# Kernel tuning notes

Hardware: AMD Instinct MI355X
Metric: run time of the kernel (lower is better)

The kernel has to match this reference:

```python
import jax, jax.numpy as jnp
import numpy as np

B, E, H, W = 8, 256, 128, 128
E0 = E1 = E2 = E3 = E // 4  # channel_split=[2,2,2,2] -> equal quarters


def _dwconv(x, w, b, dilation, padding):
    # x: [B,C,H,W], w: [C,1,kh,kw] (OIHW, feature_group_count=C), b: [C]
    C = x.shape[1]
    y = jax.lax.conv_general_dilated(
        x, w,
        window_strides=(1, 1),
        padding=[(padding, padding), (padding, padding)],
        rhs_dilation=(dilation, dilation),
        feature_group_count=C,
        dimension_numbers=("NCHW", "OIHW", "NCHW"))
    return y + b[None, :, None, None]


def setup_inputs() -> dict:
    key = jax.random.key(0)
    ks = jax.random.split(key, 9)
    s = 0.05
    return {
        "x": jax.random.normal(ks[0], (B, E, H, W), dtype=jnp.float32),
        "w0": jax.random.normal(ks[1], (E, 1, 3, 3), dtype=jnp.float32) * s,
        "b0": jax.random.normal(ks[2], (E,), dtype=jnp.float32) * s,
        "w1": jax.random.normal(ks[3], (E1, 1, 3, 3), dtype=jnp.float32) * s,
        "b1": jax.random.normal(ks[4], (E1,), dtype=jnp.float32) * s,
        "w2": jax.random.normal(ks[5], (E2, 1, 5, 5), dtype=jnp.float32) * s,
        "b2": jax.random.normal(ks[6], (E2,), dtype=jnp.float32) * s,
        "w_pw": jax.random.normal(ks[7], (E, E), dtype=jnp.float32) * s,
        "b_pw": jax.random.normal(ks[8], (E,), dtype=jnp.float32) * s,
    }


def reference(x, w0, b0, w1, b1, w2, b2, w_pw, b_pw):
    # Stage 1: full-width 3x3 depthwise, dilation 1, padding 1
    x0 = _dwconv(x, w0, b0, dilation=1, padding=1)
    # Branch convs on channel slices of x0 (note: original code applies
    # DW_conv2 to BOTH the 3rd and 4th slices; DW_conv3 is never used).
    x1 = _dwconv(x0[:, E0:E0 + E1], w1, b1, dilation=3, padding=3)          # 3x3 dil3
    x2 = _dwconv(x0[:, E0 + E1:E0 + E1 + E2], w2, b2, dilation=3, padding=6)  # 5x5 dil3
    x3 = _dwconv(x0[:, E - E3:], w2, b2, dilation=3, padding=6)             # reuses DW_conv2
    xc = jnp.concatenate([x0[:, :E0], x1, x2, x3], axis=1)  # [B,E,H,W]
    # 1x1 pointwise conv as a channel GEMM
    y = jnp.einsum("bchw,oc->bohw", xc, w_pw) + b_pw[None, :, None, None]
    return y
```

## Files before the change

kernel.cpp:

```cpp
#include <hip/hip_runtime.h>

typedef _Float16 f16;
typedef _Float16 f16x8 __attribute__((ext_vector_type(8)));
typedef unsigned short u16x8 __attribute__((ext_vector_type(8)));
typedef float f32x4 __attribute__((ext_vector_type(4)));

#define GLB_AS(p) ((const __attribute__((address_space(1))) unsigned int*)(p))
#define LDS_AS(p) ((__attribute__((address_space(3))) unsigned int*)(p))

__global__ __launch_bounds__(256) void whalf(const float* __restrict__ w,
                                             f16* __restrict__ wh) {
  int i = blockIdx.x * 256 + threadIdx.x;
  wh[i] = (f16)w[i];
}

template <int HT>
__global__ __launch_bounds__(256) void dwfuse(
    const float* __restrict__ x, const float* __restrict__ w0,
    const float* __restrict__ b0, const float* __restrict__ w1,
    const float* __restrict__ b1, const float* __restrict__ w2,
    const float* __restrict__ b2, f16* __restrict__ Xp) {
  constexpr int S2 = 32 + 2 * HT;
  constexpr int S1 = S2 + 2;
  constexpr int PO = (HT == 6) ? 2 : 0;
  constexpr int QW = (S2 + 3) / 4;
  __shared__ float xs[S1 * 48];
  __shared__ float ts[S2 * 48];
  const int tid = threadIdx.x;

  int b, ch;
  if constexpr (HT == 0) { b = blockIdx.z >> 6; ch = (int)(blockIdx.z & 63); }
  else if constexpr (HT == 3) { b = blockIdx.z >> 6; ch = 64 + (int)(blockIdx.z & 63); }
  else { b = blockIdx.z >> 7; ch = 128 + (int)(blockIdx.z & 127); }
  const int plane = b * 256 + ch;
  const int R0 = (int)blockIdx.y * 32, C0 = (int)blockIdx.x * 32;
  const float* xp = x + (size_t)plane * 16384;

  float W0[9];
#pragma unroll
  for (int k = 0; k < 9; ++k) W0[k] = w0[ch * 9 + k];
  const float B0 = b0[ch];

  const int br = R0 - HT - 1, bc = C0 - HT - 1;
  for (int i = tid; i < S1 * S1; i += 256) {
    int r = i / S1, c = i - r * S1;
    int gr = br + r, gc = bc + c;
    float v = 0.f;
    if ((unsigned)gr < 128u && (unsigned)gc < 128u) v = xp[gr * 128 + gc];
    xs[r * 48 + c] = v;
  }
  __syncthreads();

  for (int q = tid; q < S2 * QW; q += 256) {
    int r = q / QW, c4 = (q - r * QW) * 4;
    float a0 = 0, a1 = 0, a2 = 0, a3 = 0;
#pragma unroll
    for (int dy = 0; dy < 3; ++dy) {
      const float* row = &xs[(r + dy) * 48 + c4];
      float4 qa = *(const float4*)row;
      float4 qb = *(const float4*)(row + 4);
      float wA = W0[dy * 3 + 0], wB = W0[dy * 3 + 1], wC = W0[dy * 3 + 2];
      a0 += wA * qa.x + wB * qa.y + wC * qa.z;
      a1 += wA * qa.y + wB * qa.z + wC * qa.w;
      a2 += wA * qa.z + wB * qa.w + wC * qb.x;
      a3 += wA * qa.w + wB * qb.x + wC * qb.y;
    }
    int gr = R0 - HT + r;
    int gc = C0 - HT + c4;
    bool rok = (unsigned)gr < 128u;
    float o0 = (rok && (unsigned)(gc + 0) < 128u) ? a0 + B0 : 0.f;
    float o1 = (rok && (unsigned)(gc + 1) < 128u) ? a1 + B0 : 0.f;
    float o2 = (rok && (unsigned)(gc + 2) < 128u) ? a2 + B0 : 0.f;
    float o3 = (rok && (unsigned)(gc + 3) < 128u) ? a3 + B0 : 0.f;
    float* tp = &ts[r * 48 + c4 + PO];
    tp[0] = o0; tp[1] = o1; tp[2] = o2; tp[3] = o3;
  }
  __syncthreads();

  const int orow = tid >> 3;
  const int oc4 = (tid & 7) << 2;
  float o0, o1, o2, o3;
  if constexpr (HT == 0) {
    float4 qa = *(const float4*)&ts[orow * 48 + oc4];
    o0 = qa.x; o1 = qa.y; o2 = qa.z; o3 = qa.w;
  } else if constexpr (HT == 3) {
    const int wi = ch & 63;
    float W1[9];
#pragma unroll
    for (int k = 0; k < 9; ++k) W1[k] = w1[wi * 9 + k];
    o0 = o1 = o2 = o3 = b1[wi];
#pragma unroll
    for (int dy = 0; dy < 3; ++dy) {
      const float* row = &ts[(orow + 3 * dy) * 48 + oc4];
      float4 qa = *(const float4*)row;
      float4 qb = *(const float4*)(row + 4);
      float4 qc = *(const float4*)(row + 8);
      float v[12] = {qa.x, qa.y, qa.z, qa.w, qb.x, qb.y, qb.z, qb.w,
                     qc.x, qc.y, qc.z, qc.w};
#pragma unroll
      for (int dx = 0; dx < 3; ++dx) {
        float w = W1[dy * 3 + dx];
        o0 += w * v[3 * dx + 0];
        o1 += w * v[3 * dx + 1];
        o2 += w * v[3 * dx + 2];
        o3 += w * v[3 * dx + 3];
      }
    }
  } else {
    const int wi = ch & 63;
    float W2[25];
#pragma unroll
    for (int k = 0; k < 25; ++k) W2[k] = w2[wi * 25 + k];
    o0 = o1 = o2 = o3 = b2[wi];
#pragma unroll
    for (int dy = 0; dy < 5; ++dy) {
      const float* row = &ts[(orow + 3 * dy) * 48 + oc4];
      float4 qa = *(const float4*)(row + 0);
      float4 qb = *(const float4*)(row + 4);
      float4 qc = *(const float4*)(row + 8);
      float4 qd = *(const float4*)(row + 12);
      float4 qe = *(const float4*)(row + 16);
      float v[20] = {qa.x, qa.y, qa.z, qa.w, qb.x, qb.y, qb.z, qb.w,
                     qc.x, qc.y, qc.z, qc.w, qd.x, qd.y, qd.z, qd.w,
                     qe.x, qe.y, qe.z, qe.w};
#pragma unroll
      for (int dx = 0; dx < 5; ++dx) {
        float w = W2[dy * 5 + dx];
        o0 += w * v[3 * dx + 2];
        o1 += w * v[3 * dx + 3];
        o2 += w * v[3 * dx + 4];
        o3 += w * v[3 * dx + 5];
      }
    }
  }
  const size_t oidx =
      (size_t)plane * 16384 + (size_t)(R0 + orow) * 128 + (C0 + oc4);
  union { f16 h[4]; uint2 u; } ph;
  ph.h[0] = (f16)o0; ph.h[1] = (f16)o1; ph.h[2] = (f16)o2; ph.h[3] = (f16)o3;
  *(uint2*)&Xp[oidx] = ph.u;
}

__global__ __launch_bounds__(256) void t_xpose(const f16* __restrict__ Xp,
                                               f16* __restrict__ XT) {
  __shared__ unsigned ld[64 * 65];
  const int t = threadIdx.x;
  const int b = (int)blockIdx.z, c0 = (int)blockIdx.y << 6,
            p0 = (int)blockIdx.x << 6;
  {
    const int r = t >> 2, ch = (t & 3) << 4;
    const f16* src = Xp + (((size_t)b * 256 + c0 + r) << 14) + p0 + ch;
    u16x8 v0 = *(const u16x8*)src;
    u16x8 v1 = *(const u16x8*)(src + 8);
#pragma unroll
    for (int i = 0; i < 8; ++i) ld[r * 65 + ch + i] = v0[i];
#pragma unroll
    for (int i = 0; i < 8; ++i) ld[r * 65 + ch + 8 + i] = v1[i];
  }
  __syncthreads();
  {
    const int pr = t >> 2, cc = (t & 3) << 4;
    u16x8 w0, w1;
#pragma unroll
    for (int i = 0; i < 8; ++i) w0[i] = (unsigned short)ld[(cc + i) * 65 + pr];
#pragma unroll
    for (int i = 0; i < 8; ++i)
      w1[i] = (unsigned short)ld[(cc + 8 + i) * 65 + pr];
    f16* dst = XT + (((size_t)b * 16384 + p0 + pr) << 8) + c0 + cc;
    *(u16x8*)dst = w0;
    *(u16x8*)(dst + 8) = w1;
  }
}

__global__ __launch_bounds__(256) void pwgemm(const f16* __restrict__ XT,
                                              const f16* __restrict__ Wh,
                                              const float* __restrict__ bpw,
                                              float* __restrict__ out) {
  __shared__ f16 smem[4096];
  const int tid = threadIdx.x, lane = tid & 63, wid = tid >> 6;
  const int bx = (int)blockIdx.x;
  const int nblk = bx >> 1;
  const int m0 = (bx & 1) << 7;
  const int bb = nblk >> 7;
  const int p0 = (nblk & 127) << 7;

  const int sq = (tid & 3) ^ ((tid >> 2) & 3) ^ ((tid >> 4) & 3);
  const f16* xb0 =
      XT + (((size_t)bb * 16384 + p0 + (tid >> 2)) << 8) + sq * 8;
  const f16* xb1 = xb0 + (64 << 8);
  const unsigned lb0 =
      __builtin_amdgcn_readfirstlane((unsigned)(wid * 1024));
  const unsigned lb1 = lb0 + 4096;

  const int wm = (wid >> 1) << 6, wn = (wid & 1) << 6;
  const int arow = lane & 15, ak = (lane >> 4) << 3;
  const f16* wrow = Wh + (m0 + wm + arow) * 256 + ak;

  unsigned boff[4];
#pragma unroll
  for (int nf = 0; nf < 4; ++nf) {
    int px = wn + nf * 16 + (lane & 15);
    boff[nf] =
        (unsigned)(px * 64 + ((((lane >> 4) ^ px ^ (px >> 2)) & 3) << 4));
  }

  f32x4 acc[4][4] = {};
  for (int ks = 0; ks < 8; ++ks) {
    __builtin_amdgcn_global_load_lds(GLB_AS(xb0 + ks * 32),
                                     LDS_AS((char*)smem + lb0), 16, 0, 0);
    __builtin_amdgcn_global_load_lds(GLB_AS(xb1 + ks * 32),
                                     LDS_AS((char*)smem + lb1), 16, 0, 0);
    __syncthreads();

    f16x8 a[4], bfr[4];
#pragma unroll
    for (int mf = 0; mf < 4; ++mf)
      a[mf] = *(const f16x8*)(wrow + mf * 16 * 256 + ks * 32);
#pragma unroll
    for (int nf = 0; nf < 4; ++nf)
      bfr[nf] = *(const f16x8*)((const char*)smem + boff[nf]);

#pragma unroll
    for (int mf = 0; mf < 4; ++mf)
#pragma unroll
      for (int nf = 0; nf < 4; ++nf)
        acc[mf][nf] = __builtin_amdgcn_mfma_f32_16x16x32_f16(
            a[mf], bfr[nf], acc[mf][nf], 0, 0, 0);
    __syncthreads();
  }

  float brow[4][4];
#pragma unroll
  for (int mf = 0; mf < 4; ++mf)
#pragma unroll
    for (int r = 0; r < 4; ++r)
      brow[mf][r] = bpw[m0 + wm + mf * 16 + ((lane >> 4) << 2) + r];

  float* op = out + (size_t)bb * 4194304;
#pragma unroll
  for (int mf = 0; mf < 4; ++mf) {
    const int o = m0 + wm + mf * 16 + ((lane >> 4) << 2);
#pragma unroll
    for (int nf = 0; nf < 4; ++nf) {
      const int px = p0 + wn + nf * 16 + (lane & 15);
#pragma unroll
      for (int r = 0; r < 4; ++r)
        op[(size_t)(o + r) * 16384 + px] = acc[mf][nf][r] + brow[mf][r];
    }
  }
}

extern "C" void kernel_launch(void* const* d_in, const int* in_sizes, int n_in,
                              void* d_out, int out_size, void* d_ws,
                              size_t ws_size, hipStream_t stream) {
  const float* x = (const float*)d_in[0];
  const float* w0 = (const float*)d_in[1];
  const float* b0 = (const float*)d_in[2];
  const float* w1 = (const float*)d_in[3];
  const float* b1 = (const float*)d_in[4];
  const float* w2 = (const float*)d_in[5];
  const float* b2 = (const float*)d_in[6];
  const float* wpw = (const float*)d_in[7];
  const float* bpw = (const float*)d_in[8];
  float* out = (float*)d_out;

  f16* Xp = (f16*)((char*)d_out + 67108864);
  f16* XT = (f16*)d_ws;
  f16* Wh = (f16*)((char*)d_ws + 67108864);

  whalf<<<256, 256, 0, stream>>>(wpw, Wh);
  dwfuse<0><<<dim3(4, 4, 512), 256, 0, stream>>>(x, w0, b0, w1, b1, w2, b2, Xp);
  dwfuse<3><<<dim3(4, 4, 512), 256, 0, stream>>>(x, w0, b0, w1, b1, w2, b2, Xp);
  dwfuse<6><<<dim3(4, 4, 1024), 256, 0, stream>>>(x, w0, b0, w1, b1, w2, b2,
                                                  Xp);
  t_xpose<<<dim3(256, 4, 8), 256, 0, stream>>>(Xp, XT);
  pwgemm<<<2048, 256, 0, stream>>>(XT, Wh, bpw, out);
}
```

Measured before the change: 428.2 us.

## Double-buffer GEMM pixel tiles, swap MFMA operands for float4 stores, pad LDS rows

The pointwise GEMM now stages 64-channel K chunks in two LDS buffers and prefetches the next chunk while computing the current one. This halves the number of barrier pairs and overlaps global loads with MFMA work. The MFMA operand roles are swapped so pixels map to rows, which lets each lane write four contiguous pixels as one float4 store instead of scattered scalar stores. The depthwise kernel's LDS row stride goes from 48 to 52 to reduce bank conflicts. The change costs more LDS per GEMM block, which may reduce occupancy.

```diff
diff --git a/kernel.cpp b/kernel.cpp
--- a/kernel.cpp
+++ b/kernel.cpp
@@ -24,8 +24,9 @@
   constexpr int S1 = S2 + 2;
   constexpr int PO = (HT == 6) ? 2 : 0;
   constexpr int QW = (S2 + 3) / 4;
-  __shared__ float xs[S1 * 48];
-  __shared__ float ts[S2 * 48];
+  constexpr int LW = 52;
+  __shared__ float xs[S1 * LW];
+  __shared__ float ts[S2 * LW];
   const int tid = threadIdx.x;
 
   int b, ch;
@@ -47,7 +48,7 @@
     int gr = br + r, gc = bc + c;
     float v = 0.f;
     if ((unsigned)gr < 128u && (unsigned)gc < 128u) v = xp[gr * 128 + gc];
-    xs[r * 48 + c] = v;
+    xs[r * LW + c] = v;
   }
   __syncthreads();
 
@@ -56,7 +57,7 @@
     float a0 = 0, a1 = 0, a2 = 0, a3 = 0;
 #pragma unroll
     for (int dy = 0; dy < 3; ++dy) {
-      const float* row = &xs[(r + dy) * 48 + c4];
+      const float* row = &xs[(r + dy) * LW + c4];
       float4 qa = *(const float4*)row;
       float4 qb = *(const float4*)(row + 4);
       float wA = W0[dy * 3 + 0], wB = W0[dy * 3 + 1], wC = W0[dy * 3 + 2];
@@ -72,7 +73,7 @@
     float o1 = (rok && (unsigned)(gc + 1) < 128u) ? a1 + B0 : 0.f;
     float o2 = (rok && (unsigned)(gc + 2) < 128u) ? a2 + B0 : 0.f;
     float o3 = (rok && (unsigned)(gc + 3) < 128u) ? a3 + B0 : 0.f;
-    float* tp = &ts[r * 48 + c4 + PO];
+    float* tp = &ts[r * LW + c4 + PO];
     tp[0] = o0; tp[1] = o1; tp[2] = o2; tp[3] = o3;
   }
   __syncthreads();
@@ -81,7 +82,7 @@
   const int oc4 = (tid & 7) << 2;
   float o0, o1, o2, o3;
   if constexpr (HT == 0) {
-    float4 qa = *(const float4*)&ts[orow * 48 + oc4];
+    float4 qa = *(const float4*)&ts[orow * LW + oc4];
     o0 = qa.x; o1 = qa.y; o2 = qa.z; o3 = qa.w;
   } else if constexpr (HT == 3) {
     const int wi = ch & 63;
@@ -91,7 +92,7 @@
     o0 = o1 = o2 = o3 = b1[wi];
 #pragma unroll
     for (int dy = 0; dy < 3; ++dy) {
-      const float* row = &ts[(orow + 3 * dy) * 48 + oc4];
+      const float* row = &ts[(orow + 3 * dy) * LW + oc4];
       float4 qa = *(const float4*)row;
       float4 qb = *(const float4*)(row + 4);
       float4 qc = *(const float4*)(row + 8);
@@ -114,7 +115,7 @@
     o0 = o1 = o2 = o3 = b2[wi];
 #pragma unroll
     for (int dy = 0; dy < 5; ++dy) {
-      const float* row = &ts[(orow + 3 * dy) * 48 + oc4];
+      const float* row = &ts[(orow + 3 * dy) * LW + oc4];
       float4 qa = *(const float4*)(row + 0);
       float4 qb = *(const float4*)(row + 4);
       float4 qc = *(const float4*)(row + 8);
@@ -175,7 +176,7 @@
                                               const f16* __restrict__ Wh,
                                               const float* __restrict__ bpw,
                                               float* __restrict__ out) {
-  __shared__ f16 smem[4096];
+  __shared__ f16 smem[16384];
   const int tid = threadIdx.x, lane = tid & 63, wid = tid >> 6;
   const int bx = (int)blockIdx.x;
   const int nblk = bx >> 1;
@@ -183,68 +184,87 @@
   const int bb = nblk >> 7;
   const int p0 = (nblk & 127) << 7;
 
-  const int sq = (tid & 3) ^ ((tid >> 2) & 3) ^ ((tid >> 4) & 3);
-  const f16* xb0 =
-      XT + (((size_t)bb * 16384 + p0 + (tid >> 2)) << 8) + sq * 8;
-  const f16* xb1 = xb0 + (64 << 8);
-  const unsigned lb0 =
+  const int spx = tid >> 3;
+  const int so = (tid & 7) ^ (spx & 7);
+  const f16* xb = XT + (((size_t)bb * 16384 + p0 + spx) << 8) + so * 8;
+  const unsigned lwb =
       __builtin_amdgcn_readfirstlane((unsigned)(wid * 1024));
-  const unsigned lb1 = lb0 + 4096;
-
-  const int wm = (wid >> 1) << 6, wn = (wid & 1) << 6;
-  const int arow = lane & 15, ak = (lane >> 4) << 3;
-  const f16* wrow = Wh + (m0 + wm + arow) * 256 + ak;
-
-  unsigned boff[4];
-#pragma unroll
-  for (int nf = 0; nf < 4; ++nf) {
-    int px = wn + nf * 16 + (lane & 15);
-    boff[nf] =
-        (unsigned)(px * 64 + ((((lane >> 4) ^ px ^ (px >> 2)) & 3) << 4));
+
+  const int wo = (wid >> 1) << 6, wp = (wid & 1) << 6;
+  const int brow_ = lane & 15, boct = lane >> 4;
+  const f16* wrow = Wh + (m0 + wo + brow_) * 256 + boct * 8;
+
+  unsigned aoff[4][2];
+#pragma unroll
+  for (int mf = 0; mf < 4; ++mf) {
+    int px = wp + mf * 16 + (lane & 15);
+#pragma unroll
+    for (int k2 = 0; k2 < 2; ++k2)
+      aoff[mf][k2] =
+          (unsigned)(px * 128 + ((((k2 << 2) + boct) ^ (px & 7)) << 4));
   }
 
   f32x4 acc[4][4] = {};
-  for (int ks = 0; ks < 8; ++ks) {
-    __builtin_amdgcn_global_load_lds(GLB_AS(xb0 + ks * 32),
-                                     LDS_AS((char*)smem + lb0), 16, 0, 0);
-    __builtin_amdgcn_global_load_lds(GLB_AS(xb1 + ks * 32),
-                                     LDS_AS((char*)smem + lb1), 16, 0, 0);
+
+#pragma unroll
+  for (int rnd = 0; rnd < 4; ++rnd)
+    __builtin_amdgcn_global_load_lds(
+        GLB_AS(xb + rnd * 8192),
+        LDS_AS((char*)smem + rnd * 4096 + lwb), 16, 0, 0);
+  __syncthreads();
+
+  for (int ks = 0; ks < 4; ++ks) {
+    const int cur = ks & 1;
+    if (ks < 3) {
+#pragma unroll
+      for (int rnd = 0; rnd < 4; ++rnd)
+        __builtin_amdgcn_global_load_lds(
+            GLB_AS(xb + rnd * 8192 + (ks + 1) * 64),
+            LDS_AS((char*)smem + (cur ^ 1) * 16384 + rnd * 4096 + lwb), 16, 0,
+            0);
+    }
+    f16x8 bw[4][2], ax[4][2];
+#pragma unroll
+    for (int nf = 0; nf < 4; ++nf)
+#pragma unroll
+      for (int k2 = 0; k2 < 2; ++k2)
+        bw[nf][k2] = *(const f16x8*)(wrow + nf * 16 * 256 + ks * 64 + k2 * 32);
+#pragma unroll
+    for (int mf = 0; mf < 4; ++mf)
+#pragma unroll
+      for (int k2 = 0; k2 < 2; ++k2)
+        ax[mf][k2] =
+            *(const f16x8*)((const char*)smem + cur * 16384 + aoff[mf][k2]);
+
+#pragma unroll
+    for (int k2 = 0; k2 < 2; ++k2)
+#pragma unroll
+      for (int mf = 0; mf < 4; ++mf)
+#pragma unroll
+        for (int nf = 0; nf < 4; ++nf)
+          acc[mf][nf] = __builtin_amdgcn_mfma_f32_16x16x32_f16(
+              ax[mf][k2], bw[nf][k2], acc[mf][nf], 0, 0, 0);
     __syncthreads();
-
-    f16x8 a[4], bfr[4];
-#pragma unroll
-    for (int mf = 0; mf < 4; ++mf)
-      a[mf] = *(const f16x8*)(wrow + mf * 16 * 256 + ks * 32);
-#pragma unroll
-    for (int nf = 0; nf < 4; ++nf)
-      bfr[nf] = *(const f16x8*)((const char*)smem + boff[nf]);
-
-#pragma unroll
-    for (int mf = 0; mf < 4; ++mf)
-#pragma unroll
-      for (int nf = 0; nf < 4; ++nf)
-        acc[mf][nf] = __builtin_amdgcn_mfma_f32_16x16x32_f16(
-            a[mf], bfr[nf], acc[mf][nf], 0, 0, 0);
-    __syncthreads();
-  }
-
-  float brow[4][4];
-#pragma unroll
-  for (int mf = 0; mf < 4; ++mf)
-#pragma unroll
-    for (int r = 0; r < 4; ++r)
-      brow[mf][r] = bpw[m0 + wm + mf * 16 + ((lane >> 4) << 2) + r];
+  }
+
+  float bias_o[4];
+#pragma unroll
+  for (int nf = 0; nf < 4; ++nf)
+    bias_o[nf] = bpw[m0 + wo + nf * 16 + (lane & 15)];
 
   float* op = out + (size_t)bb * 4194304;
+  const int px0 = p0 + wp + ((lane >> 4) << 2);
 #pragma unroll
   for (int mf = 0; mf < 4; ++mf) {
-    const int o = m0 + wm + mf * 16 + ((lane >> 4) << 2);
 #pragma unroll
     for (int nf = 0; nf < 4; ++nf) {
-      const int px = p0 + wn + nf * 16 + (lane & 15);
-#pragma unroll
-      for (int r = 0; r < 4; ++r)
-        op[(size_t)(o + r) * 16384 + px] = acc[mf][nf][r] + brow[mf][r];
+      const int o = m0 + wo + nf * 16 + (lane & 15);
+      float4 v;
+      v.x = acc[mf][nf][0] + bias_o[nf];
+      v.y = acc[mf][nf][1] + bias_o[nf];
+      v.z = acc[mf][nf][2] + bias_o[nf];
+      v.w = acc[mf][nf][3] + bias_o[nf];
+      *(float4*)&op[(size_t)o * 16384 + px0 + mf * 16] = v;
     }
   }
 }
```

Result: no change. 425.7 us (-0.6%).
